# Kernel optimization log

Measured on AMD Instinct MI355X. Metric: run time of the kernel, lower is better.

Reference implementation:

```python
import jax, jax.numpy as jnp
import numpy as np

N_WAY = 5
K_SHOT = 5
TEMPERATURE = 1.0
NEG = -1e9  # emulates 'column does not exist' for pad columns beyond umask_length
EPS = 1e-12  # matches torch F.normalize eps


def _l2n(x, axis):
    n = jnp.sqrt(jnp.sum(x * x, axis=axis, keepdims=True))
    return x / jnp.maximum(n, EPS)


def setup_inputs() -> dict:
    key = jax.random.key(0)
    k1, k2, k3, k4, k5 = jax.random.split(key, 5)
    b, c, h, w = 4, 64, 5, 5
    q, u = 75, 100
    support_xf = jax.random.normal(k1, (b, N_WAY * K_SHOT, c, h, w), jnp.float32)
    query_xf = jax.random.normal(k2, (b, q, c, h, w), jnp.float32)
    unlabeled_xf = jax.random.normal(k3, (b, u, c, h, w), jnp.float32)
    support_y = jax.random.randint(k4, (b, N_WAY * K_SHOT), 0, N_WAY)
    query_y = jax.random.randint(k5, (b, q), 0, N_WAY)
    return {"support_xf": support_xf, "support_y": support_y, "query_xf": query_xf,
            "query_y": query_y, "unlabeled_xf": unlabeled_xf}


def _forward(support_xf, query_xf, unlabeled_xf, query_y):
    b, q, c, h, w = query_xf.shape
    M_s = K_SHOT * h * w
    unl = unlabeled_xf.reshape(b, -1, c, h, w)
    u = unl.shape[1]
    M_u = u * h * w
    # pooled unlabeled local descriptors, flattened in (u, h, w) order -> [b, c, M_u]
    unl_feat = unl.transpose(0, 2, 1, 3, 4).reshape(b, c, M_u)
    # support -> [b, n_way, c, k_shot*h*w]
    sup = support_xf.reshape(b, N_WAY, K_SHOT, c, h, w).transpose(0, 1, 3, 2, 4, 5).reshape(b, N_WAY, c, M_s)
    # cosine similarity unlabeled -> support: [b, n_way, M_u, M_s]
    u2s = jnp.einsum('bwcn,bcm->bwmn', _l2n(sup, 2), _l2n(unl_feat, 1))
    pool = u2s.transpose(0, 2, 1, 3).reshape(b, M_u, N_WAY * M_s)
    s_nearest = jnp.argmax(pool, axis=1)          # per support loc: nearest unlabeled loc
    u_nearest = jnp.argmax(pool, axis=2)          # per unlabeled loc: nearest support loc
    mutual = jnp.take_along_axis(s_nearest, u_nearest, axis=1) == jnp.arange(M_u)[None, :]  # [b, M_u]
    # class with max similarity per unlabeled location
    cls = jnp.argmax(jnp.max(u2s, axis=-1), axis=1)  # [b, M_u]
    umask = jax.nn.one_hot(cls, N_WAY, dtype=jnp.float32).transpose(0, 2, 1) \
            * mutual[:, None, :].astype(jnp.float32)  # [b, n_way, M_u]
    counts = umask.sum(-1)                          # [b, n_way]
    L = counts.max()                                # umask_length (traced)
    # stream compaction via stable argsort of the 0/1 mask (preserves original order)
    order = jnp.argsort(-umask, axis=-1)            # jnp.argsort is stable
    pts = unl_feat.transpose(0, 2, 1)               # [b, M_u, c]
    gath = jnp.take_along_axis(pts[:, None, :, :], order[..., None], axis=2)  # [b, n_way, M_u, c]
    valid = (jnp.arange(M_u)[None, None, :] < counts[:, :, None]).astype(jnp.float32)
    comp = gath * valid[..., None]                  # rows beyond count are zeros (as in torch)
    s_cat = jnp.concatenate([sup, comp.transpose(0, 1, 3, 2)], axis=-1)  # [b, n_way, c, M_s+M_u]
    M_tot = M_s + M_u
    qn = _l2n(query_xf.reshape(b, q, c, h * w), 2)
    scn = _l2n(s_cat, 2)
    sim = jnp.einsum('bqcm,bwcn->bqwmn', qn, scn)   # [b, q, n_way, M_q, M_tot]
    sim = (sim + 1.0) * 0.5                          # FourLayer_64F branch
    # columns beyond umask_length don't exist in the torch dense tensor -> exclude from maxes
    pad = jnp.arange(M_tot)[None, None, None, None, :] >= (M_s + L)
    sim = jnp.where(pad, NEG, sim)
    M_q = h * w
    qm = sim.transpose(0, 1, 3, 2, 4).reshape(b, q, M_q, N_WAY * M_tot)
    support_nearest = jnp.argmax(qm, axis=2)        # [b, q, n_way*M_tot]
    query_nearest = jnp.argmax(qm, axis=3)          # [b, q, M_q]
    g = jnp.take_along_axis(support_nearest, query_nearest, axis=2)
    q_mask = (g == jnp.arange(M_q)[None, None, :]).astype(sim.dtype)  # mutual NN mask
    query_value = (jnp.max(sim, axis=-1) * q_mask[:, :, None, :]).sum(-1)  # [b, q, n_way]
    logits = query_value.reshape(b * q, N_WAY) / TEMPERATURE
    y = query_y.reshape(b * q)
    logp = jax.nn.log_softmax(logits, axis=-1)
    loss = -jnp.take_along_axis(logp, y[:, None], axis=1).mean()
    return loss


def reference(support_xf, support_y, query_xf, query_y, unlabeled_xf):
    return _forward(support_xf, query_xf, unlabeled_xf, query_y)
```

## Files before the change

kernel.cpp:

```cpp
#include <hip/hip_runtime.h>

#define NEGINF (-1e30f)

constexpr size_t OF_UNL  = 0;
constexpr size_t OF_SUP  = OF_UNL  + (size_t)4*2500*64;
constexpr size_t OF_SUPT = OF_SUP  + (size_t)4*5*125*64;
constexpr size_t OF_QT   = OF_SUPT + (size_t)4*5*64*128;
constexpr size_t OF_ROWV = OF_QT   + (size_t)300*64*25;
constexpr size_t OF_ROWI = OF_ROWV + (size_t)4*5*8*2500;
constexpr size_t OF_CVI  = OF_ROWI + (size_t)4*5*8*2500;
constexpr size_t OF_CMP  = OF_CVI  + (size_t)4*5*125*20*2;
constexpr size_t OF_CNT  = OF_CMP  + (size_t)4*5*2500;
constexpr size_t OF_UNEAR= OF_CNT  + 20;
constexpr size_t OF_SNEAR= OF_UNEAR+ 10000;
constexpr size_t OF_BV   = OF_SNEAR+ 2500;
constexpr size_t OF_BP   = OF_BV   + 37500;
constexpr size_t OF_AMX  = OF_BP   + 37500;

__global__ __launch_bounds__(256) void knorm(
    const float* __restrict__ sup, const float* __restrict__ qry,
    const float* __restrict__ unl,
    float* __restrict__ unl_n, float* __restrict__ sup_n,
    float* __restrict__ supT, float* __restrict__ qt)
{
    int gid = blockIdx.x * 256 + threadIdx.x;
    int loc = gid >> 4;
    int sub = gid & 15;
    if (loc >= 20000) return;

    const float* src;
    float* dst1;
    float* dst2 = nullptr;

    if (loc < 10000) {
        int b = loc / 2500, m = loc % 2500;
        int u = m / 25, hw = m % 25;
        src  = unl + ((size_t)(b*100 + u) * 64) * 25 + hw;
        dst1 = unl_n + (size_t)loc * 64;
    } else if (loc < 12500) {
        int idx = loc - 10000;
        int b = idx / 625, r = idx % 625;
        int w = r / 125,  n = r % 125;
        int shot = n / 25, hw = n % 25;
        src  = sup + ((size_t)(b*25 + w*5 + shot) * 64) * 25 + hw;
        dst1 = sup_n + (size_t)idx * 64;
        dst2 = supT + ((size_t)(b*5 + w) * 64) * 128 + n;
    } else {
        int idx = loc - 12500;
        int bq = idx / 25, mq = idx % 25;
        src  = qry + ((size_t)bq * 64) * 25 + mq;
        dst1 = qt + ((size_t)bq * 25 + mq) * 64;
    }

    float v[4]; float ss = 0.f;
    int c0 = sub * 4;
#pragma unroll
    for (int j = 0; j < 4; ++j) { v[j] = src[(size_t)(c0 + j) * 25]; ss += v[j] * v[j]; }
#pragma unroll
    for (int msk = 1; msk < 16; msk <<= 1) ss += __shfl_xor(ss, msk);
    float sc = 1.f / fmaxf(sqrtf(ss), 1e-12f);
#pragma unroll
    for (int j = 0; j < 4; ++j) {
        float o = v[j] * sc;
        dst1[c0 + j] = o;
        if (dst2) dst2[(size_t)(c0 + j) * 128] = o;
    }
}

__global__ __launch_bounds__(256) void kb(
    const float* __restrict__ unl_n, const float* __restrict__ supT,
    float* __restrict__ rowv, int* __restrict__ rowi, float* __restrict__ colvi)
{
    int bid = blockIdx.x;
    int nc = bid & 3;
    int mb = (bid >> 2) % 20;
    int bw = bid / 80;
    int b  = bw / 5;
    int tid = threadIdx.x;
    int lane = tid & 63, wv = tid >> 6;

    __shared__ float uls[128 * 65];
    __shared__ float sls[64 * 36];
    __shared__ float sv_[4][32];
    __shared__ int   si_[4][32];

    int m0 = mb * 128;
    int n0 = nc * 32;

    for (int i = tid; i < 128 * 16; i += 256) {
        int row = i >> 4, c4 = (i & 15) * 4;
        int m = m0 + row;
        float4 x = make_float4(0.f, 0.f, 0.f, 0.f);
        if (m < 2500) x = *(const float4*)(unl_n + ((size_t)(b * 2500 + m)) * 64 + c4);
        uls[row * 65 + c4 + 0] = x.x;
        uls[row * 65 + c4 + 1] = x.y;
        uls[row * 65 + c4 + 2] = x.z;
        uls[row * 65 + c4 + 3] = x.w;
    }
    {
        int c = tid >> 2, q = tid & 3;
        const float* sp = supT + ((size_t)bw * 64 + c) * 128 + n0 + q * 8;
        float4 a = *(const float4*)sp;
        float4 d4 = *(const float4*)(sp + 4);
        float* d = &sls[c * 36 + q * 8];
        d[0] = a.x; d[1] = a.y; d[2] = a.z; d[3] = a.w;
        d[4] = d4.x; d[5] = d4.y; d[6] = d4.z; d[7] = d4.w;
    }
    __syncthreads();

    int ml = tid & 127;
    int m  = m0 + ml;
    int nh = tid >> 7;
    int nbase = nh * 16;
    int nn_total = (125 - n0) < 32 ? (125 - n0) : 32;
    const float* myrow = &uls[ml * 65];

    float acc[16];
#pragma unroll
    for (int j = 0; j < 16; ++j) acc[j] = 0.f;

    for (int c = 0; c < 64; ++c) {
        float uv = myrow[c];
        const float4* sr = (const float4*)&sls[c * 36 + nbase];
        float4 s0 = sr[0], s1 = sr[1], s2 = sr[2], s3 = sr[3];
        acc[0]  = fmaf(uv, s0.x, acc[0]);  acc[1]  = fmaf(uv, s0.y, acc[1]);
        acc[2]  = fmaf(uv, s0.z, acc[2]);  acc[3]  = fmaf(uv, s0.w, acc[3]);
        acc[4]  = fmaf(uv, s1.x, acc[4]);  acc[5]  = fmaf(uv, s1.y, acc[5]);
        acc[6]  = fmaf(uv, s1.z, acc[6]);  acc[7]  = fmaf(uv, s1.w, acc[7]);
        acc[8]  = fmaf(uv, s2.x, acc[8]);  acc[9]  = fmaf(uv, s2.y, acc[9]);
        acc[10] = fmaf(uv, s2.z, acc[10]); acc[11] = fmaf(uv, s2.w, acc[11]);
        acc[12] = fmaf(uv, s3.x, acc[12]); acc[13] = fmaf(uv, s3.y, acc[13]);
        acc[14] = fmaf(uv, s3.z, acc[14]); acc[15] = fmaf(uv, s3.w, acc[15]);
    }

    int nnloc = nn_total - nbase;
    nnloc = nnloc < 0 ? 0 : (nnloc > 16 ? 16 : nnloc);
    float rbv = NEGINF; int rbi = 0;
    for (int j = 0; j < nnloc; ++j)
        if (acc[j] > rbv) { rbv = acc[j]; rbi = n0 + nbase + j; }
    if (m < 2500) {
        int ck = nc * 2 + nh;
        rowv[((size_t)bw * 8 + ck) * 2500 + m] = rbv;
        rowi[((size_t)bw * 8 + ck) * 2500 + m] = rbi;
    }

#pragma unroll
    for (int j = 0; j < 16; ++j) {
        float v = (m < 2500 && (nbase + j) < nn_total) ? acc[j] : NEGINF;
        float vm = v;
#pragma unroll
        for (int s2 = 1; s2 < 64; s2 <<= 1) vm = fmaxf(vm, __shfl_xor(vm, s2));
        unsigned long long msk = __ballot(v == vm);
        int first = __ffsll((unsigned long long)msk) - 1;
        if (lane == 0) { sv_[wv][nbase + j] = vm; si_[wv][nbase + j] = m0 + (wv & 1) * 64 + first; }
    }
    __syncthreads();
    if (tid < nn_total) {
        int w0 = (tid < 16) ? 0 : 2;
        float v = sv_[w0][tid];     int vi = si_[w0][tid];
        float v2 = sv_[w0 + 1][tid]; int i2 = si_[w0 + 1][tid];
        if (v2 > v || (v2 == v && i2 < vi)) { v = v2; vi = i2; }
        float* cv = colvi + ((((size_t)bw) * 125 + (n0 + tid)) * 20 + mb) * 2;
        cv[0] = v; ((int*)cv)[1] = vi;
    }
}

__global__ __launch_bounds__(256) void kmerge(
    const float* __restrict__ rowv, const int* __restrict__ rowi,
    const float* __restrict__ colvi,
    int* __restrict__ unear, int* __restrict__ snear)
{
    int it = blockIdx.x * 256 + threadIdx.x;
    if (it < 10000) {
        int b = it / 2500, m = it % 2500;
        float bv = NEGINF; int bi = 0;
#pragma unroll
        for (int w = 0; w < 5; ++w) {
#pragma unroll
            for (int ck = 0; ck < 8; ++ck) {
                size_t o = (((size_t)(b * 5 + w)) * 8 + ck) * 2500 + m;
                float v = rowv[o];
                if (v > bv) { bv = v; bi = w * 125 + rowi[o]; }
            }
        }
        unear[it] = bi;
    } else if (it < 12500) {
        int idx = it - 10000;
        const float* p = colvi + (size_t)idx * 40;
        float bv = NEGINF; int bi = 0x7fffffff;
        for (int mb2 = 0; mb2 < 20; ++mb2) {
            float v = p[mb2 * 2]; int vi = ((const int*)p)[mb2 * 2 + 1];
            if (v > bv || (v == bv && vi < bi)) { bv = v; bi = vi; }
        }
        snear[idx] = bi;
    }
}

__global__ __launch_bounds__(256) void kcmp(
    const int* __restrict__ unear, const int* __restrict__ snear,
    int* __restrict__ cmp, int* __restrict__ cntg)
{
    int p = blockIdx.x;
    int b = p / 5, way = p % 5;
    int tid = threadIdx.x, lane = tid & 63, wv = tid >> 6;
    __shared__ unsigned long long masks[40];
    __shared__ int base[40];

    for (int ch = wv; ch < 40; ch += 4) {
        int m = ch * 64 + lane;
        bool ok = false;
        if (m < 2500) {
            int un = unear[b * 2500 + m];
            ok = (un / 125 == way) && (snear[b * 625 + un] == m);
        }
        unsigned long long msk = __ballot(ok ? 1 : 0);
        if (lane == 0) masks[ch] = msk;
    }
    __syncthreads();
    if (tid == 0) {
        int s = 0;
        for (int ch = 0; ch < 40; ++ch) { base[ch] = s; s += __popcll(masks[ch]); }
        cntg[p] = s;
    }
    __syncthreads();
    for (int ch = wv; ch < 40; ch += 4) {
        unsigned long long msk = masks[ch];
        if ((msk >> lane) & 1ull) {
            int pre = __popcll(msk & ((1ull << lane) - 1ull));
            cmp[(size_t)p * 2500 + base[ch] + pre] = ch * 64 + lane;
        }
    }
}

__global__ __launch_bounds__(256) void kc1(
    const float* __restrict__ qt, const float* __restrict__ sup_n,
    const float* __restrict__ unl_n, const int* __restrict__ cmp,
    const int* __restrict__ cntg,
    float* __restrict__ bvg, int* __restrict__ bpg,
    unsigned char* __restrict__ amaxg)
{
    int bid = blockIdx.x;
    int w = bid % 5, bq = bid / 5;
    int b = bq / 75;
    int tid = threadIdx.x;

    const float* qtb = qt + (size_t)bq * 1600;

    int L = 0;
#pragma unroll
    for (int i = 0; i < 20; ++i) { int v = cntg[i]; L = L > v ? L : v; }
    int cntw = 0, wb = 0;
#pragma unroll
    for (int w2 = 0; w2 < 5; ++w2) {
        int c2 = cntg[b * 5 + w2];
        if (w2 < w) wb += 125 + c2;
        if (w2 == w) cntw = c2;
    }
    int cw = 125 + cntw;

    __shared__ float qls[25 * 64];
    __shared__ float simb[25 * 257];
    __shared__ float redv[8][25];
    __shared__ int   redp[8][25];

    for (int i = tid; i < 1600; i += 256) qls[i] = qtb[i];

    int rg = tid / 25, rq = tid % 25;
    float bv1 = NEGINF; int bp1 = 0x7fffffff;
    __syncthreads();

    for (int c0 = 0; c0 < cw; c0 += 256) {
        int n = c0 + tid;
        if (n < cw) {
            const float* colp;
            if (n < 125) colp = sup_n + (((size_t)(b * 5 + w)) * 125 + n) * 64;
            else {
                int m = cmp[((size_t)(b * 5 + w)) * 2500 + (n - 125)];
                colp = unl_n + ((size_t)(b * 2500 + m)) * 64;
            }
            float acc[25];
#pragma unroll
            for (int i = 0; i < 25; ++i) acc[i] = 0.f;
#pragma unroll
            for (int cg = 0; cg < 16; ++cg) {
                float4 cv = *(const float4*)(colp + cg * 4);
#pragma unroll
                for (int mq = 0; mq < 25; ++mq) {
                    float4 qv = *(const float4*)&qls[mq * 64 + cg * 4];
                    acc[mq] = fmaf(cv.x, qv.x, acc[mq]);
                    acc[mq] = fmaf(cv.y, qv.y, acc[mq]);
                    acc[mq] = fmaf(cv.z, qv.z, acc[mq]);
                    acc[mq] = fmaf(cv.w, qv.w, acc[mq]);
                }
            }
            float cmax = NEGINF; int cam = 0;
#pragma unroll
            for (int mq = 0; mq < 25; ++mq) {
                float s = (acc[mq] + 1.0f) * 0.5f;
                if (s > cmax) { cmax = s; cam = mq; }
                simb[mq * 257 + tid] = s;
            }
            amaxg[(size_t)bq * 3200 + (wb + n)] = (unsigned char)cam;
        }
        __syncthreads();
        if (tid < 200) {
            int base = rg * 32;
            for (int i = 0; i < 32; ++i) {
                int n2 = c0 + base + i;
                if (n2 < cw) {
                    float s = simb[rq * 257 + base + i];
                    if (s > bv1) { bv1 = s; bp1 = ((w * 2625 + n2) << 12) | (wb + n2); }
                }
            }
        }
        __syncthreads();
    }

    if (tid < 200) { redv[rg][rq] = bv1; redp[rg][rq] = bp1; }
    __syncthreads();
    if (tid < 25) {
        float v = redv[0][tid]; int p = redp[0][tid];
#pragma unroll
        for (int g = 1; g < 8; ++g)
            if (redv[g][tid] > v) { v = redv[g][tid]; p = redp[g][tid]; }
        if (L > cntw) {
            int pp = ((w * 2625 + 125 + cntw) << 12) | 0xFFF;
            if (0.5f > v || (0.5f == v && pp < p)) { v = 0.5f; p = pp; }
        }
        size_t o = ((size_t)bq * 5 + w) * 25 + tid;
        bvg[o] = v; bpg[o] = p;
    }
}

__global__ __launch_bounds__(64) void kce(
    const float* __restrict__ bvg, const int* __restrict__ bpg,
    const unsigned char* __restrict__ amaxg, const int* __restrict__ qy,
    float* __restrict__ out)
{
    int bq = blockIdx.x;
    int tid = threadIdx.x;
    __shared__ float qmask[25];
    __shared__ float lg[5];
    if (tid < 25) {
        float v = NEGINF; int p = 0x7fffffff;
#pragma unroll
        for (int w = 0; w < 5; ++w) {
            size_t o = ((size_t)bq * 5 + w) * 25 + tid;
            float v2 = bvg[o]; int p2 = bpg[o];
            if (v2 > v || (v2 == v && p2 < p)) { v = v2; p = p2; }
        }
        int pos = p & 0xFFF;
        int g = (pos == 0xFFF) ? 0 : (int)amaxg[(size_t)bq * 3200 + pos];
        qmask[tid] = (g == tid) ? 1.0f : 0.0f;
    }
    __syncthreads();
    if (tid < 5) {
        float s = 0.f;
#pragma unroll
        for (int mq = 0; mq < 25; ++mq)
            s += bvg[((size_t)bq * 5 + tid) * 25 + mq] * qmask[mq];
        lg[tid] = s;
    }
    __syncthreads();
    if (tid == 0) {
        int y = qy[bq];
        float mx = lg[0];
#pragma unroll
        for (int w = 1; w < 5; ++w) mx = fmaxf(mx, lg[w]);
        float se = 0.f;
#pragma unroll
        for (int w = 0; w < 5; ++w) se += expf(lg[w] - mx);
        float loss = -(lg[y] - mx - logf(se));
        atomicAdd(out, loss * (1.0f / 300.0f));
    }
}

extern "C" void kernel_launch(void* const* d_in, const int* in_sizes, int n_in,
                              void* d_out, int out_size, void* d_ws, size_t ws_size,
                              hipStream_t stream)
{
    const float* sup = (const float*)d_in[0];
    const float* qry = (const float*)d_in[2];
    const int*   qy  = (const int*)d_in[3];
    const float* unl = (const float*)d_in[4];

    float* ws    = (float*)d_ws;
    float* unl_n = ws + OF_UNL;
    float* sup_n = ws + OF_SUP;
    float* supT  = ws + OF_SUPT;
    float* qt    = ws + OF_QT;
    float* rowv  = ws + OF_ROWV;
    int*   rowi  = (int*)(ws + OF_ROWI);
    float* colvi = ws + OF_CVI;
    int*   cmp   = (int*)(ws + OF_CMP);
    int*   cntg  = (int*)(ws + OF_CNT);
    int*   unear = (int*)(ws + OF_UNEAR);
    int*   snear = (int*)(ws + OF_SNEAR);
    float* bvg   = ws + OF_BV;
    int*   bpg   = (int*)(ws + OF_BP);
    unsigned char* amaxg = (unsigned char*)(ws + OF_AMX);

    hipMemsetAsync(d_out, 0, sizeof(float), stream);

    hipLaunchKernelGGL(knorm, dim3(1250), dim3(256), 0, stream,
                       sup, qry, unl, unl_n, sup_n, supT, qt);
    hipLaunchKernelGGL(kb, dim3(1600), dim3(256), 0, stream,
                       unl_n, supT, rowv, rowi, colvi);
    hipLaunchKernelGGL(kmerge, dim3(49), dim3(256), 0, stream,
                       rowv, rowi, colvi, unear, snear);
    hipLaunchKernelGGL(kcmp, dim3(20), dim3(256), 0, stream,
                       unear, snear, cmp, cntg);
    hipLaunchKernelGGL(kc1, dim3(1500), dim3(256), 0, stream,
                       qt, sup_n, unl_n, cmp, cntg, bvg, bpg, amaxg);
    hipLaunchKernelGGL(kce, dim3(300), dim3(64), 0, stream,
                       bvg, bpg, amaxg, qy, (float*)d_out);
}
```

Baseline: 184.7 us.

## Read query descriptors from global in channel-group layout, drop LDS staging and column loop

The normalization kernel now writes query descriptors in a channel-group-major layout (groups of 4 channels × 25 locations), so the similarity kernel can read them directly from global memory as wave-uniform float4 loads instead of staging them into shared memory. The outer column loop is removed on the assumption that each class has at most 256 columns (125 support plus mutual unlabeled), which drops one round of barriers. Out-of-range threads clamp their column index and compute redundantly. This is correct only if cw never exceeds 256, and it relies on cache or scalar-load behavior for the repeated global reads of query data.

```diff
diff --git a/kernel.cpp b/kernel.cpp
--- a/kernel.cpp
+++ b/kernel.cpp
@@ -29,8 +29,9 @@
     if (loc >= 20000) return;
 
     const float* src;
-    float* dst1;
+    float* dst1; int q_mode = 0;
     float* dst2 = nullptr;
+    int qmq = 0;
 
     if (loc < 10000) {
         int b = loc / 2500, m = loc % 2500;
@@ -47,9 +48,10 @@
         dst2 = supT + ((size_t)(b*5 + w) * 64) * 128 + n;
     } else {
         int idx = loc - 12500;
-        int bq = idx / 25, mq = idx % 25;
-        src  = qry + ((size_t)bq * 64) * 25 + mq;
-        dst1 = qt + ((size_t)bq * 25 + mq) * 64;
+        int bq = idx / 25; qmq = idx % 25;
+        src  = qry + ((size_t)bq * 64) * 25 + qmq;
+        dst1 = qt + (size_t)bq * 1600;
+        q_mode = 1;
     }
 
     float v[4]; float ss = 0.f;
@@ -62,7 +64,8 @@
 #pragma unroll
     for (int j = 0; j < 4; ++j) {
         float o = v[j] * sc;
-        dst1[c0 + j] = o;
+        if (q_mode) dst1[sub * 100 + qmq * 4 + j] = o;
+        else        dst1[c0 + j] = o;
         if (dst2) dst2[(size_t)(c0 + j) * 128] = o;
     }
 }
@@ -258,65 +261,59 @@
     }
     int cw = 125 + cntw;
 
-    __shared__ float qls[25 * 64];
     __shared__ float simb[25 * 257];
     __shared__ float redv[8][25];
     __shared__ int   redp[8][25];
 
-    for (int i = tid; i < 1600; i += 256) qls[i] = qtb[i];
-
     int rg = tid / 25, rq = tid % 25;
     float bv1 = NEGINF; int bp1 = 0x7fffffff;
-    __syncthreads();
-
-    for (int c0 = 0; c0 < cw; c0 += 256) {
-        int n = c0 + tid;
-        if (n < cw) {
-            const float* colp;
-            if (n < 125) colp = sup_n + (((size_t)(b * 5 + w)) * 125 + n) * 64;
-            else {
-                int m = cmp[((size_t)(b * 5 + w)) * 2500 + (n - 125)];
-                colp = unl_n + ((size_t)(b * 2500 + m)) * 64;
+
+    {
+        int n = tid;
+        int nn = n < cw ? n : cw - 1;
+        const float* colp;
+        if (nn < 125) colp = sup_n + (((size_t)(b * 5 + w)) * 125 + nn) * 64;
+        else {
+            int m = cmp[((size_t)(b * 5 + w)) * 2500 + (nn - 125)];
+            colp = unl_n + ((size_t)(b * 2500 + m)) * 64;
+        }
+        float acc[25];
+#pragma unroll
+        for (int i = 0; i < 25; ++i) acc[i] = 0.f;
+#pragma unroll
+        for (int cg = 0; cg < 16; ++cg) {
+            float4 cv = *(const float4*)(colp + cg * 4);
+            const float* qcg = qtb + cg * 100;
+#pragma unroll
+            for (int mq = 0; mq < 25; ++mq) {
+                float4 qv = *(const float4*)(qcg + mq * 4);
+                acc[mq] = fmaf(cv.x, qv.x, acc[mq]);
+                acc[mq] = fmaf(cv.y, qv.y, acc[mq]);
+                acc[mq] = fmaf(cv.z, qv.z, acc[mq]);
+                acc[mq] = fmaf(cv.w, qv.w, acc[mq]);
             }
-            float acc[25];
-#pragma unroll
-            for (int i = 0; i < 25; ++i) acc[i] = 0.f;
-#pragma unroll
-            for (int cg = 0; cg < 16; ++cg) {
-                float4 cv = *(const float4*)(colp + cg * 4);
-#pragma unroll
-                for (int mq = 0; mq < 25; ++mq) {
-                    float4 qv = *(const float4*)&qls[mq * 64 + cg * 4];
-                    acc[mq] = fmaf(cv.x, qv.x, acc[mq]);
-                    acc[mq] = fmaf(cv.y, qv.y, acc[mq]);
-                    acc[mq] = fmaf(cv.z, qv.z, acc[mq]);
-                    acc[mq] = fmaf(cv.w, qv.w, acc[mq]);
-                }
+        }
+        float cmax = NEGINF; int cam = 0;
+#pragma unroll
+        for (int mq = 0; mq < 25; ++mq) {
+            float s = (acc[mq] + 1.0f) * 0.5f;
+            if (s > cmax) { cmax = s; cam = mq; }
+            if (n < cw) simb[mq * 257 + tid] = s;
+        }
+        if (n < cw) amaxg[(size_t)bq * 3200 + (wb + n)] = (unsigned char)cam;
+    }
+    __syncthreads();
+    if (tid < 200) {
+        int base = rg * 32;
+        for (int i = 0; i < 32; ++i) {
+            int n2 = base + i;
+            if (n2 < cw) {
+                float s = simb[rq * 257 + n2];
+                if (s > bv1) { bv1 = s; bp1 = ((w * 2625 + n2) << 12) | (wb + n2); }
             }
-            float cmax = NEGINF; int cam = 0;
-#pragma unroll
-            for (int mq = 0; mq < 25; ++mq) {
-                float s = (acc[mq] + 1.0f) * 0.5f;
-                if (s > cmax) { cmax = s; cam = mq; }
-                simb[mq * 257 + tid] = s;
-            }
-            amaxg[(size_t)bq * 3200 + (wb + n)] = (unsigned char)cam;
-        }
-        __syncthreads();
-        if (tid < 200) {
-            int base = rg * 32;
-            for (int i = 0; i < 32; ++i) {
-                int n2 = c0 + base + i;
-                if (n2 < cw) {
-                    float s = simb[rq * 257 + base + i];
-                    if (s > bv1) { bv1 = s; bp1 = ((w * 2625 + n2) << 12) | (wb + n2); }
-                }
-            }
-        }
-        __syncthreads();
-    }
-
-    if (tid < 200) { redv[rg][rq] = bv1; redp[rg][rq] = bp1; }
+        }
+        redv[rg][rq] = bv1; redp[rg][rq] = bp1;
+    }
     __syncthreads();
     if (tid < 25) {
         float v = redv[0][tid]; int p = redp[0][tid];
```

New measurement: 256.4 us. 38.8% more time.

## Register-tile kc1 similarity as 4 columns x 5 query rows per thread

Applied to the files above, without the earlier changes.

Rewrites the query-to-support similarity kernel so each of 320 threads computes a 5x4 register tile: 5 waves each own 5 query rows and each lane owns 4 columns. It processes all columns in one pass, which relies on the column count never exceeding 256. The row-max and column-argmax reductions move into a separate phase over shared memory. The intent is more reuse of each LDS query load and column load per FMA, fewer barriers, and no loop over column chunks. The trade-off is a larger block and the single-pass bound on column count.

```diff
diff --git a/kernel.cpp b/kernel.cpp
--- a/kernel.cpp
+++ b/kernel.cpp
@@ -232,7 +232,7 @@
     }
 }
 
-__global__ __launch_bounds__(256) void kc1(
+__global__ __launch_bounds__(320) void kc1(
     const float* __restrict__ qt, const float* __restrict__ sup_n,
     const float* __restrict__ unl_n, const int* __restrict__ cmp,
     const int* __restrict__ cntg,
@@ -243,8 +243,7 @@
     int w = bid % 5, bq = bid / 5;
     int b = bq / 75;
     int tid = threadIdx.x;
-
-    const float* qtb = qt + (size_t)bq * 1600;
+    int lane = tid & 63, ty = tid >> 6;
 
     int L = 0;
 #pragma unroll
@@ -259,69 +258,87 @@
     int cw = 125 + cntw;
 
     __shared__ float qls[25 * 64];
-    __shared__ float simb[25 * 257];
-    __shared__ float redv[8][25];
-    __shared__ int   redp[8][25];
-
-    for (int i = tid; i < 1600; i += 256) qls[i] = qtb[i];
-
-    int rg = tid / 25, rq = tid % 25;
-    float bv1 = NEGINF; int bp1 = 0x7fffffff;
-    __syncthreads();
-
-    for (int c0 = 0; c0 < cw; c0 += 256) {
-        int n = c0 + tid;
-        if (n < cw) {
-            const float* colp;
-            if (n < 125) colp = sup_n + (((size_t)(b * 5 + w)) * 125 + n) * 64;
-            else {
-                int m = cmp[((size_t)(b * 5 + w)) * 2500 + (n - 125)];
-                colp = unl_n + ((size_t)(b * 2500 + m)) * 64;
+    __shared__ float simb[25 * 260];
+    __shared__ float redv[10][25];
+    __shared__ int   redp[10][25];
+
+    for (int i = tid; i < 1600; i += 320) qls[i] = qt[(size_t)bq * 1600 + i];
+
+    int col0 = lane * 4;
+    const float* colp0; const float* colp1; const float* colp2; const float* colp3;
+    {
+        const int* cmpw = cmp + ((size_t)(b * 5 + w)) * 2500;
+#define COLPTR(J, DST) { int n = col0 + (J); n = n < cw ? n : cw - 1; \
+        if (n < 125) DST = sup_n + (((size_t)(b * 5 + w)) * 125 + n) * 64; \
+        else DST = unl_n + ((size_t)(b * 2500 + cmpw[n - 125])) * 64; }
+        COLPTR(0, colp0) COLPTR(1, colp1) COLPTR(2, colp2) COLPTR(3, colp3)
+#undef COLPTR
+    }
+    __syncthreads();
+
+    float acc[5][4];
+#pragma unroll
+    for (int i = 0; i < 5; ++i)
+#pragma unroll
+        for (int j = 0; j < 4; ++j) acc[i][j] = 0.f;
+
+    const float* qbase = &qls[ty * 5 * 64];
+    for (int cg = 0; cg < 16; ++cg) {
+        float4 cv0 = *(const float4*)(colp0 + cg * 4);
+        float4 cv1 = *(const float4*)(colp1 + cg * 4);
+        float4 cv2 = *(const float4*)(colp2 + cg * 4);
+        float4 cv3 = *(const float4*)(colp3 + cg * 4);
+#pragma unroll
+        for (int i = 0; i < 5; ++i) {
+            float4 qv = *(const float4*)(qbase + i * 64 + cg * 4);
+            acc[i][0] = fmaf(cv0.x, qv.x, fmaf(cv0.y, qv.y, fmaf(cv0.z, qv.z, fmaf(cv0.w, qv.w, acc[i][0]))));
+            acc[i][1] = fmaf(cv1.x, qv.x, fmaf(cv1.y, qv.y, fmaf(cv1.z, qv.z, fmaf(cv1.w, qv.w, acc[i][1]))));
+            acc[i][2] = fmaf(cv2.x, qv.x, fmaf(cv2.y, qv.y, fmaf(cv2.z, qv.z, fmaf(cv2.w, qv.w, acc[i][2]))));
+            acc[i][3] = fmaf(cv3.x, qv.x, fmaf(cv3.y, qv.y, fmaf(cv3.z, qv.z, fmaf(cv3.w, qv.w, acc[i][3]))));
+        }
+    }
+
+#pragma unroll
+    for (int i = 0; i < 5; ++i) {
+        float4 sv;
+        sv.x = (acc[i][0] + 1.0f) * 0.5f;
+        sv.y = (acc[i][1] + 1.0f) * 0.5f;
+        sv.z = (acc[i][2] + 1.0f) * 0.5f;
+        sv.w = (acc[i][3] + 1.0f) * 0.5f;
+        *(float4*)&simb[(ty * 5 + i) * 260 + col0] = sv;
+    }
+    __syncthreads();
+
+    if (tid < 256) {
+        int col = tid;
+        if (col < cw) {
+            float cmax = NEGINF; int cam = 0;
+#pragma unroll
+            for (int mq = 0; mq < 25; ++mq) {
+                float s = simb[mq * 260 + col];
+                if (s > cmax) { cmax = s; cam = mq; }
             }
-            float acc[25];
-#pragma unroll
-            for (int i = 0; i < 25; ++i) acc[i] = 0.f;
-#pragma unroll
-            for (int cg = 0; cg < 16; ++cg) {
-                float4 cv = *(const float4*)(colp + cg * 4);
-#pragma unroll
-                for (int mq = 0; mq < 25; ++mq) {
-                    float4 qv = *(const float4*)&qls[mq * 64 + cg * 4];
-                    acc[mq] = fmaf(cv.x, qv.x, acc[mq]);
-                    acc[mq] = fmaf(cv.y, qv.y, acc[mq]);
-                    acc[mq] = fmaf(cv.z, qv.z, acc[mq]);
-                    acc[mq] = fmaf(cv.w, qv.w, acc[mq]);
-                }
+            amaxg[(size_t)bq * 3200 + (wb + col)] = (unsigned char)cam;
+        }
+    }
+    if (tid < 250) {
+        int rg = tid / 25, rq = tid % 25;
+        float bv1 = NEGINF; int bp1 = 0x7fffffff;
+        int base = rg * 25;
+        for (int i = 0; i < 25; ++i) {
+            int col = base + i;
+            if (col < cw) {
+                float s = simb[rq * 260 + col];
+                if (s > bv1) { bv1 = s; bp1 = ((w * 2625 + col) << 12) | (wb + col); }
             }
-            float cmax = NEGINF; int cam = 0;
-#pragma unroll
-            for (int mq = 0; mq < 25; ++mq) {
-                float s = (acc[mq] + 1.0f) * 0.5f;
-                if (s > cmax) { cmax = s; cam = mq; }
-                simb[mq * 257 + tid] = s;
-            }
-            amaxg[(size_t)bq * 3200 + (wb + n)] = (unsigned char)cam;
-        }
-        __syncthreads();
-        if (tid < 200) {
-            int base = rg * 32;
-            for (int i = 0; i < 32; ++i) {
-                int n2 = c0 + base + i;
-                if (n2 < cw) {
-                    float s = simb[rq * 257 + base + i];
-                    if (s > bv1) { bv1 = s; bp1 = ((w * 2625 + n2) << 12) | (wb + n2); }
-                }
-            }
-        }
-        __syncthreads();
-    }
-
-    if (tid < 200) { redv[rg][rq] = bv1; redp[rg][rq] = bp1; }
+        }
+        redv[rg][rq] = bv1; redp[rg][rq] = bp1;
+    }
     __syncthreads();
     if (tid < 25) {
         float v = redv[0][tid]; int p = redp[0][tid];
 #pragma unroll
-        for (int g = 1; g < 8; ++g)
+        for (int g = 1; g < 10; ++g)
             if (redv[g][tid] > v) { v = redv[g][tid]; p = redp[g][tid]; }
         if (L > cntw) {
             int pp = ((w * 2625 + 125 + cntw) << 12) | 0xFFF;
@@ -410,7 +427,7 @@
                        rowv, rowi, colvi, unear, snear);
     hipLaunchKernelGGL(kcmp, dim3(20), dim3(256), 0, stream,
                        unear, snear, cmp, cntg);
-    hipLaunchKernelGGL(kc1, dim3(1500), dim3(256), 0, stream,
+    hipLaunchKernelGGL(kc1, dim3(1500), dim3(320), 0, stream,
                        qt, sup_n, unl_n, cmp, cntg, bvg, bpg, amaxg);
     hipLaunchKernelGGL(kce, dim3(300), dim3(64), 0, stream,
                        bvg, bpg, amaxg, qy, (float*)d_out);
```

Measured after the change: 220.9 us. 19.6% more time.
